# Kernel tuning notes

Measured on AMD Instinct MI355X. Metric: run time of the kernel, lower is better.

The kernel has to match this reference:

```python
import jax, jax.numpy as jnp
import numpy as np

B, N, N_IN, MSG_HID, MSG_OUT, N_HID, N_OUT, K = 32, 128, 16, 64, 64, 64, 16, 4
E = N * (N - 1)  # 16256 directed edges, fully connected w/o self-loops


def setup_inputs() -> dict:
    key = jax.random.key(0)
    ks = jax.random.split(key, 8)
    # one-hot relation matrices (NRI convention)
    rows, cols = np.where(np.ones((N, N)) - np.eye(N))
    eye = np.eye(N, dtype=np.float32)
    rel_rec = jnp.asarray(eye[rows])   # [E, N]
    rel_send = jnp.asarray(eye[cols])  # [E, N]
    s = 0.1  # weight init scale
    return {
        "inputs": jax.random.normal(ks[0], (B, N_IN, N), jnp.float32),
        "rel_rec": rel_rec,
        "rel_send": rel_send,
        "rel_types": jax.nn.softmax(jax.random.normal(ks[1], (B, E, K), jnp.float32), axis=-1),
        "W1": jax.random.normal(ks[2], (K, 2 * N_IN, MSG_HID), jnp.float32) * s,
        "b1": jnp.zeros((K, MSG_HID), jnp.float32),
        "W2": jax.random.normal(ks[3], (K, MSG_HID, MSG_OUT), jnp.float32) * s,
        "b2": jnp.zeros((K, MSG_OUT), jnp.float32),
        "Wo1": jax.random.normal(ks[4], (MSG_OUT + N_IN, N_HID), jnp.float32) * s,
        "bo1": jnp.zeros((N_HID,), jnp.float32),
        "Wo2": jax.random.normal(ks[5], (N_HID, N_HID), jnp.float32) * s,
        "bo2": jnp.zeros((N_HID,), jnp.float32),
        "Wo3": jax.random.normal(ks[6], (N_HID, N_OUT), jnp.float32) * s,
        "bo3": jnp.zeros((N_OUT,), jnp.float32),
    }


def reference(inputs, rel_rec, rel_send, rel_types, W1, b1, W2, b2, Wo1, bo1, Wo2, bo2, Wo3, bo3):
    x = jnp.transpose(inputs, (0, 2, 1))                     # [B, N, n_in]
    senders = jnp.einsum('en,bnf->bef', rel_send, x)          # [B, E, n_in]
    receivers = jnp.einsum('en,bnf->bef', rel_rec, x)         # [B, E, n_in]
    pre_msg = jnp.concatenate([senders, receivers], axis=-1)  # [B, E, 2*n_in]
    all_msgs = jnp.zeros((pre_msg.shape[0], pre_msg.shape[1], W2.shape[-1]), pre_msg.dtype)
    for k in range(W1.shape[0]):  # small fixed loop over edge types
        m = jax.nn.relu(pre_msg @ W1[k] + b1[k])
        m = jax.nn.relu(m @ W2[k] + b2[k])
        all_msgs = all_msgs + m * rel_types[:, :, k:k + 1]
    # edge2node aggregation (no normalization in forward path, matches source)
    agg_msgs = jnp.einsum('bem,en->bnm', all_msgs, rel_rec)   # [B, N, msg_out]
    aug_msgs = jnp.concatenate([x, agg_msgs], axis=-1)        # [B, N, n_in+msg_out]
    h = jax.nn.relu(aug_msgs @ Wo1 + bo1)  # dropout disabled (eval mode)
    h = jax.nn.relu(h @ Wo2 + bo2)
    pred = h @ Wo3 + bo3                                      # [B, N, n_out]
    return jnp.transpose(pred, (0, 2, 1))                     # [B, n_out, N]
```

## Files before the change

kernel.cpp:

```cpp
#include <hip/hip_runtime.h>
#include <stdint.h>

#define B_  32
#define N_  128
#define NIN 16
#define K_  4
#define E_  (N_*(N_-1))

typedef float f4   __attribute__((ext_vector_type(4)));
typedef short bf8  __attribute__((ext_vector_type(8)));

static __device__ __forceinline__ unsigned short f2bf(float f) {
    union { float f; unsigned u; } v; v.f = f;
    unsigned r = v.u + 0x7FFFu + ((v.u >> 16) & 1u);
    return (unsigned short)(r >> 16);
}
static __device__ __forceinline__ float bf2f(unsigned short h) {
    union { unsigned u; float f; } v; v.u = ((unsigned)h) << 16;
    return v.f;
}

__global__ __launch_bounds__(256) void precompute_sr(
    const float* __restrict__ inp, const float* __restrict__ W1,
    const float* __restrict__ b1,
    unsigned short* __restrict__ Sb, unsigned short* __restrict__ Rb)
{
    int gid = blockIdx.x * 256 + threadIdx.x;
    int c = gid & 63;
    int n = (gid >> 6) & 127;
    int b = (gid >> 13) & 31;
    int k = gid >> 18;
    float s = 0.f, r = 0.f;
    const float* w1s = W1 + (k*32)*64 + c;
    const float* w1r = W1 + (k*32 + 16)*64 + c;
    const float* xp  = inp + (b*NIN)*N_ + n;
    #pragma unroll
    for (int f = 0; f < 16; ++f) {
        float xv = xp[f*N_];
        s += xv * w1s[f*64];
        r += xv * w1r[f*64];
    }
    r += b1[k*64 + c];
    Sb[gid] = f2bf(s);
    Rb[gid] = f2bf(r);
}

__global__ __launch_bounds__(256) void pack_w2(
    const float* __restrict__ W2, unsigned short* __restrict__ w2b)
{
    int t = blockIdx.x * 256 + threadIdx.x;
    int i    = t & 7;
    int lane = (t >> 3) & 63;
    int nt   = (t >> 9) & 3;
    int ks   = (t >> 11) & 1;
    int k    = t >> 12;
    int c = ks*32 + (lane >> 4)*8 + i;
    int o = nt*16 + (lane & 15);
    w2b[t] = f2bf(W2[(k*64 + c)*64 + o]);
}

__global__ __launch_bounds__(256) void edge_node(
    const unsigned short* __restrict__ Sb,
    const unsigned short* __restrict__ Rb,
    const unsigned short* __restrict__ w2b,
    const float* __restrict__ inp,
    const float* __restrict__ rt,
    const float* __restrict__ b2,
    const float* __restrict__ Wo1, const float* __restrict__ bo1,
    const float* __restrict__ Wo2, const float* __restrict__ bo2,
    const float* __restrict__ Wo3, const float* __restrict__ bo3,
    float* __restrict__ out)
{
    __shared__ float aggK[4*64];
    __shared__ float aug[80];
    __shared__ float h1s[64];
    __shared__ float h2s[64];

    const int tid  = threadIdx.x;
    const int r    = blockIdx.x & 127;
    const int b    = blockIdx.x >> 7;
    const int k    = tid >> 6;
    const int lane = tid & 63;
    const int col  = lane & 15;
    const int q    = lane >> 4;

    if (tid < 16) aug[tid] = inp[(b*NIN + tid)*N_ + r];

    const bf8* w2v = (const bf8*)w2b;
    bf8 w2f[2][4];
    #pragma unroll
    for (int ks = 0; ks < 2; ++ks)
        #pragma unroll
        for (int nt = 0; nt < 4; ++nt)
            w2f[ks][nt] = w2v[((k*2 + ks)*4 + nt)*64 + lane];

    const bf8* Sv = (const bf8*)Sb;
    const bf8* Rv = (const bf8*)Rb;
    const int rowbaseR = ((k*B_ + b)*N_ + r) * 8;
    float rf[2][8];
    #pragma unroll
    for (int ks = 0; ks < 2; ++ks) {
        bf8 rv = Rv[rowbaseR + ks*4 + q];
        #pragma unroll
        for (int i = 0; i < 8; ++i) rf[ks][i] = bf2f((unsigned short)rv[i]);
    }

    float b2v[4];
    #pragma unroll
    for (int nt = 0; nt < 4; ++nt) b2v[nt] = b2[k*64 + nt*16 + col];

    float aggacc[4] = {0.f, 0.f, 0.f, 0.f};
    const int rowbaseS = (k*B_ + b)*N_*8;
    const int ebase    = b*E_ + r*127;

    for (int mt = 0; mt < 8; ++mt) {
        int j = mt*16 + col;
        int s = j + (j >= r ? 1 : 0);
        if (s > 127) s = 127;
        bf8 h1f[2];
        #pragma unroll
        for (int ks = 0; ks < 2; ++ks) {
            bf8 sv = Sv[rowbaseS + s*8 + ks*4 + q];
            bf8 h;
            #pragma unroll
            for (int i = 0; i < 8; ++i) {
                float v = bf2f((unsigned short)sv[i]) + rf[ks][i];
                h[i] = (short)f2bf(fmaxf(v, 0.f));
            }
            h1f[ks] = h;
        }
        f4 acc[4];
        #pragma unroll
        for (int nt = 0; nt < 4; ++nt) {
            f4 z = {0.f, 0.f, 0.f, 0.f};
            acc[nt] = __builtin_amdgcn_mfma_f32_16x16x32_bf16(h1f[0], w2f[0][nt], z, 0, 0, 0);
            acc[nt] = __builtin_amdgcn_mfma_f32_16x16x32_bf16(h1f[1], w2f[1][nt], acc[nt], 0, 0, 0);
        }
        float rtv[4];
        #pragma unroll
        for (int i = 0; i < 4; ++i) {
            int jrow = mt*16 + q*4 + i;
            rtv[i] = (jrow < 127) ? rt[(ebase + jrow)*4 + k] : 0.f;
        }
        #pragma unroll
        for (int nt = 0; nt < 4; ++nt)
            #pragma unroll
            for (int i = 0; i < 4; ++i)
                aggacc[nt] += rtv[i] * fmaxf(acc[nt][i] + b2v[nt], 0.f);
    }

    #pragma unroll
    for (int nt = 0; nt < 4; ++nt) {
        float v = aggacc[nt];
        v += __shfl_xor(v, 16, 64);
        v += __shfl_xor(v, 32, 64);
        if (lane < 16) aggK[k*64 + nt*16 + lane] = v;
    }
    __syncthreads();

    if (tid < 64) {
        float a = aggK[tid] + aggK[64 + tid] + aggK[128 + tid] + aggK[192 + tid];
        aug[16 + tid] = a;
    }
    __syncthreads();
    if (tid < 64) {
        float accv = bo1[tid];
        #pragma unroll 8
        for (int i = 0; i < 80; ++i) accv += aug[i] * Wo1[i*64 + tid];
        h1s[tid] = fmaxf(accv, 0.f);
    }
    __syncthreads();
    if (tid < 64) {
        float accv = bo2[tid];
        #pragma unroll 8
        for (int i = 0; i < 64; ++i) accv += h1s[i] * Wo2[i*64 + tid];
        h2s[tid] = fmaxf(accv, 0.f);
    }
    __syncthreads();
    if (tid < 16) {
        float accv = bo3[tid];
        #pragma unroll 8
        for (int i = 0; i < 64; ++i) accv += h2s[i] * Wo3[i*16 + tid];
        out[(b*NIN + tid)*N_ + r] = accv;
    }
}

extern "C" void kernel_launch(void* const* d_in, const int* in_sizes, int n_in,
                              void* d_out, int out_size, void* d_ws, size_t ws_size,
                              hipStream_t stream)
{
    const float* inp = (const float*)d_in[0];
    const float* rt  = (const float*)d_in[3];
    const float* W1  = (const float*)d_in[4];
    const float* b1  = (const float*)d_in[5];
    const float* W2  = (const float*)d_in[6];
    const float* b2  = (const float*)d_in[7];
    const float* Wo1 = (const float*)d_in[8];
    const float* bo1 = (const float*)d_in[9];
    const float* Wo2 = (const float*)d_in[10];
    const float* bo2 = (const float*)d_in[11];
    const float* Wo3 = (const float*)d_in[12];
    const float* bo3 = (const float*)d_in[13];

    unsigned short* Sb  = (unsigned short*)d_ws;
    unsigned short* Rb  = Sb + (1u << 20);
    unsigned short* w2b = Rb + (1u << 20);

    hipLaunchKernelGGL(precompute_sr, dim3(4096), dim3(256), 0, stream,
                       inp, W1, b1, Sb, Rb);
    hipLaunchKernelGGL(pack_w2, dim3(64), dim3(256), 0, stream, W2, w2b);
    hipLaunchKernelGGL(edge_node, dim3(B_*N_), dim3(256), 0, stream,
                       Sb, Rb, w2b, inp, rt, b2,
                       Wo1, bo1, Wo2, bo2, Wo3, bo3, (float*)d_out);
}
```

Before: 166.2 us.

## Switch to fp16 MFMA, fuse prep kernels, transpose rel_types, split node MLP

```diff
diff --git a/kernel.cpp b/kernel.cpp
--- a/kernel.cpp
+++ b/kernel.cpp
@@ -7,65 +7,63 @@
 #define K_  4
 #define E_  (N_*(N_-1))
 
-typedef float f4   __attribute__((ext_vector_type(4)));
-typedef short bf8  __attribute__((ext_vector_type(8)));
-
-static __device__ __forceinline__ unsigned short f2bf(float f) {
-    union { float f; unsigned u; } v; v.f = f;
-    unsigned r = v.u + 0x7FFFu + ((v.u >> 16) & 1u);
-    return (unsigned short)(r >> 16);
+typedef float    f4 __attribute__((ext_vector_type(4)));
+typedef _Float16 h8 __attribute__((ext_vector_type(8)));
+
+__global__ __launch_bounds__(256) void prep(
+    const float* __restrict__ inp, const float* __restrict__ W1,
+    const float* __restrict__ b1,  const float* __restrict__ W2,
+    const float* __restrict__ rt,
+    _Float16* __restrict__ Sh, _Float16* __restrict__ Rh,
+    _Float16* __restrict__ w2h, float* __restrict__ rtp)
+{
+    const int bid = blockIdx.x;
+    const int tid = threadIdx.x;
+    if (bid < 4096) {
+        int gid = bid*256 + tid;
+        int c = gid & 63;
+        int n = (gid >> 6) & 127;
+        int b = (gid >> 13) & 31;
+        int k = gid >> 18;
+        float s = 0.f, r = 0.f;
+        const float* w1s = W1 + (k*32)*64 + c;
+        const float* w1r = W1 + (k*32 + 16)*64 + c;
+        const float* xp  = inp + (b*NIN)*N_ + n;
+        #pragma unroll
+        for (int f = 0; f < 16; ++f) {
+            float xv = xp[f*N_];
+            s += xv * w1s[f*64];
+            r += xv * w1r[f*64];
+        }
+        r += b1[k*64 + c];
+        Sh[gid] = (_Float16)s;
+        Rh[gid] = (_Float16)r;
+    } else if (bid < 4160) {
+        int t = (bid - 4096)*256 + tid;
+        int i    = t & 7;
+        int lane = (t >> 3) & 63;
+        int nt   = (t >> 9) & 3;
+        int ks   = (t >> 11) & 1;
+        int k    = t >> 12;
+        int c = ks*32 + (lane >> 4)*8 + i;
+        int o = nt*16 + (lane & 15);
+        w2h[t] = (_Float16)W2[(k*64 + c)*64 + o];
+    } else {
+        int t = (bid - 4160)*256 + tid;
+        int j = t & 127;
+        int r = (t >> 7) & 127;
+        int b = (t >> 14) & 31;
+        int k = t >> 19;
+        float v = 0.f;
+        if (j < 127) v = rt[(b*E_ + r*127 + j)*4 + k];
+        rtp[t] = v;
+    }
 }
-static __device__ __forceinline__ float bf2f(unsigned short h) {
-    union { unsigned u; float f; } v; v.u = ((unsigned)h) << 16;
-    return v.f;
-}
-
-__global__ __launch_bounds__(256) void precompute_sr(
-    const float* __restrict__ inp, const float* __restrict__ W1,
-    const float* __restrict__ b1,
-    unsigned short* __restrict__ Sb, unsigned short* __restrict__ Rb)
-{
-    int gid = blockIdx.x * 256 + threadIdx.x;
-    int c = gid & 63;
-    int n = (gid >> 6) & 127;
-    int b = (gid >> 13) & 31;
-    int k = gid >> 18;
-    float s = 0.f, r = 0.f;
-    const float* w1s = W1 + (k*32)*64 + c;
-    const float* w1r = W1 + (k*32 + 16)*64 + c;
-    const float* xp  = inp + (b*NIN)*N_ + n;
-    #pragma unroll
-    for (int f = 0; f < 16; ++f) {
-        float xv = xp[f*N_];
-        s += xv * w1s[f*64];
-        r += xv * w1r[f*64];
-    }
-    r += b1[k*64 + c];
-    Sb[gid] = f2bf(s);
-    Rb[gid] = f2bf(r);
-}
-
-__global__ __launch_bounds__(256) void pack_w2(
-    const float* __restrict__ W2, unsigned short* __restrict__ w2b)
-{
-    int t = blockIdx.x * 256 + threadIdx.x;
-    int i    = t & 7;
-    int lane = (t >> 3) & 63;
-    int nt   = (t >> 9) & 3;
-    int ks   = (t >> 11) & 1;
-    int k    = t >> 12;
-    int c = ks*32 + (lane >> 4)*8 + i;
-    int o = nt*16 + (lane & 15);
-    w2b[t] = f2bf(W2[(k*64 + c)*64 + o]);
-}
 
 __global__ __launch_bounds__(256) void edge_node(
-    const unsigned short* __restrict__ Sb,
-    const unsigned short* __restrict__ Rb,
-    const unsigned short* __restrict__ w2b,
-    const float* __restrict__ inp,
-    const float* __restrict__ rt,
-    const float* __restrict__ b2,
+    const _Float16* __restrict__ Sh, const _Float16* __restrict__ Rh,
+    const _Float16* __restrict__ w2h, const float* __restrict__ rtp,
+    const float* __restrict__ inp, const float* __restrict__ b2,
     const float* __restrict__ Wo1, const float* __restrict__ bo1,
     const float* __restrict__ Wo2, const float* __restrict__ bo2,
     const float* __restrict__ Wo3, const float* __restrict__ bo3,
@@ -73,6 +71,7 @@
 {
     __shared__ float aggK[4*64];
     __shared__ float aug[80];
+    __shared__ float psum[4][64];
     __shared__ float h1s[64];
     __shared__ float h2s[64];
 
@@ -86,67 +85,52 @@
 
     if (tid < 16) aug[tid] = inp[(b*NIN + tid)*N_ + r];
 
-    const bf8* w2v = (const bf8*)w2b;
-    bf8 w2f[2][4];
+    const h8* w2v = (const h8*)w2h;
+    h8 w2f[2][4];
     #pragma unroll
     for (int ks = 0; ks < 2; ++ks)
         #pragma unroll
         for (int nt = 0; nt < 4; ++nt)
             w2f[ks][nt] = w2v[((k*2 + ks)*4 + nt)*64 + lane];
 
-    const bf8* Sv = (const bf8*)Sb;
-    const bf8* Rv = (const bf8*)Rb;
-    const int rowbaseR = ((k*B_ + b)*N_ + r) * 8;
-    float rf[2][8];
-    #pragma unroll
-    for (int ks = 0; ks < 2; ++ks) {
-        bf8 rv = Rv[rowbaseR + ks*4 + q];
-        #pragma unroll
-        for (int i = 0; i < 8; ++i) rf[ks][i] = bf2f((unsigned short)rv[i]);
-    }
-
-    float b2v[4];
-    #pragma unroll
-    for (int nt = 0; nt < 4; ++nt) b2v[nt] = b2[k*64 + nt*16 + col];
+    const h8* Sv = (const h8*)Sh;
+    const h8* Rv = (const h8*)Rh;
+    const int rowR = ((k*B_ + b)*N_ + r) * 8;
+    h8 rf0 = Rv[rowR + q];
+    h8 rf1 = Rv[rowR + 4 + q];
+
+    f4 b2i[4];
+    #pragma unroll
+    for (int nt = 0; nt < 4; ++nt) {
+        float v = b2[k*64 + nt*16 + col];
+        b2i[nt][0] = v; b2i[nt][1] = v; b2i[nt][2] = v; b2i[nt][3] = v;
+    }
 
     float aggacc[4] = {0.f, 0.f, 0.f, 0.f};
-    const int rowbaseS = (k*B_ + b)*N_*8;
-    const int ebase    = b*E_ + r*127;
-
+    const int rowSbase = (k*B_ + b)*N_*8;
+    const float* rtrow = rtp + ((k*B_ + b)*N_ + r)*128;
+    const h8 zero8 = {0,0,0,0,0,0,0,0};
+
+    #pragma unroll
     for (int mt = 0; mt < 8; ++mt) {
         int j = mt*16 + col;
         int s = j + (j >= r ? 1 : 0);
         if (s > 127) s = 127;
-        bf8 h1f[2];
-        #pragma unroll
-        for (int ks = 0; ks < 2; ++ks) {
-            bf8 sv = Sv[rowbaseS + s*8 + ks*4 + q];
-            bf8 h;
-            #pragma unroll
-            for (int i = 0; i < 8; ++i) {
-                float v = bf2f((unsigned short)sv[i]) + rf[ks][i];
-                h[i] = (short)f2bf(fmaxf(v, 0.f));
-            }
-            h1f[ks] = h;
-        }
-        f4 acc[4];
+        h8 a0 = Sv[rowSbase + s*8 + q]     + rf0;
+        h8 a1 = Sv[rowSbase + s*8 + 4 + q] + rf1;
+        a0 = __builtin_elementwise_max(a0, zero8);
+        a1 = __builtin_elementwise_max(a1, zero8);
+
+        f4 rtv = *(const f4*)(rtrow + mt*16 + q*4);
+
         #pragma unroll
         for (int nt = 0; nt < 4; ++nt) {
-            f4 z = {0.f, 0.f, 0.f, 0.f};
-            acc[nt] = __builtin_amdgcn_mfma_f32_16x16x32_bf16(h1f[0], w2f[0][nt], z, 0, 0, 0);
-            acc[nt] = __builtin_amdgcn_mfma_f32_16x16x32_bf16(h1f[1], w2f[1][nt], acc[nt], 0, 0, 0);
-        }
-        float rtv[4];
-        #pragma unroll
-        for (int i = 0; i < 4; ++i) {
-            int jrow = mt*16 + q*4 + i;
-            rtv[i] = (jrow < 127) ? rt[(ebase + jrow)*4 + k] : 0.f;
-        }
-        #pragma unroll
-        for (int nt = 0; nt < 4; ++nt)
+            f4 acc = __builtin_amdgcn_mfma_f32_16x16x32_f16(a0, w2f[0][nt], b2i[nt], 0, 0, 0);
+            acc     = __builtin_amdgcn_mfma_f32_16x16x32_f16(a1, w2f[1][nt], acc,    0, 0, 0);
             #pragma unroll
             for (int i = 0; i < 4; ++i)
-                aggacc[nt] += rtv[i] * fmaxf(acc[nt][i] + b2v[nt], 0.f);
+                aggacc[nt] += rtv[i] * fmaxf(acc[i], 0.f);
+        }
     }
 
     #pragma unroll
@@ -158,31 +142,45 @@
     }
     __syncthreads();
 
+    if (tid < 64)
+        aug[16 + tid] = aggK[tid] + aggK[64 + tid] + aggK[128 + tid] + aggK[192 + tid];
+    __syncthreads();
+
+    {
+        int o = tid & 63, p = tid >> 6;
+        float s = 0.f;
+        #pragma unroll
+        for (int i = p*20; i < p*20 + 20; ++i) s += aug[i] * Wo1[i*64 + o];
+        psum[p][o] = s;
+    }
+    __syncthreads();
+    if (tid < 64)
+        h1s[tid] = fmaxf(psum[0][tid] + psum[1][tid] + psum[2][tid] + psum[3][tid] + bo1[tid], 0.f);
+    __syncthreads();
+
+    {
+        int o = tid & 63, p = tid >> 6;
+        float s = 0.f;
+        #pragma unroll
+        for (int i = p*16; i < p*16 + 16; ++i) s += h1s[i] * Wo2[i*64 + o];
+        psum[p][o] = s;
+    }
+    __syncthreads();
+    if (tid < 64)
+        h2s[tid] = fmaxf(psum[0][tid] + psum[1][tid] + psum[2][tid] + psum[3][tid] + bo2[tid], 0.f);
+    __syncthreads();
+
     if (tid < 64) {
-        float a = aggK[tid] + aggK[64 + tid] + aggK[128 + tid] + aggK[192 + tid];
-        aug[16 + tid] = a;
-    }
-    __syncthreads();
-    if (tid < 64) {
-        float accv = bo1[tid];
-        #pragma unroll 8
-        for (int i = 0; i < 80; ++i) accv += aug[i] * Wo1[i*64 + tid];
-        h1s[tid] = fmaxf(accv, 0.f);
-    }
-    __syncthreads();
-    if (tid < 64) {
-        float accv = bo2[tid];
-        #pragma unroll 8
-        for (int i = 0; i < 64; ++i) accv += h1s[i] * Wo2[i*64 + tid];
-        h2s[tid] = fmaxf(accv, 0.f);
-    }
-    __syncthreads();
-    if (tid < 16) {
-        float accv = bo3[tid];
-        #pragma unroll 8
-        for (int i = 0; i < 64; ++i) accv += h2s[i] * Wo3[i*16 + tid];
-        out[(b*NIN + tid)*N_ + r] = accv;
-    }
+        int o = tid & 15, p = tid >> 4;
+        float s = 0.f;
+        #pragma unroll
+        for (int i = p*16; i < p*16 + 16; ++i) s += h2s[i] * Wo3[i*16 + o];
+        psum[p][o] = s;
+    }
+    __syncthreads();
+    if (tid < 16)
+        out[(b*NIN + tid)*N_ + r] =
+            psum[0][tid] + psum[1][tid] + psum[2][tid] + psum[3][tid] + bo3[tid];
 }
 
 extern "C" void kernel_launch(void* const* d_in, const int* in_sizes, int n_in,
@@ -202,14 +200,14 @@
     const float* Wo3 = (const float*)d_in[12];
     const float* bo3 = (const float*)d_in[13];
 
-    unsigned short* Sb  = (unsigned short*)d_ws;
-    unsigned short* Rb  = Sb + (1u << 20);
-    unsigned short* w2b = Rb + (1u << 20);
-
-    hipLaunchKernelGGL(precompute_sr, dim3(4096), dim3(256), 0, stream,
-                       inp, W1, b1, Sb, Rb);
-    hipLaunchKernelGGL(pack_w2, dim3(64), dim3(256), 0, stream, W2, w2b);
+    _Float16* Sh  = (_Float16*)d_ws;
+    _Float16* Rh  = Sh + (1u << 20);
+    _Float16* w2h = Rh + (1u << 20);
+    float*    rtp = (float*)(w2h + 16384);
+
+    hipLaunchKernelGGL(prep, dim3(12352), dim3(256), 0, stream,
+                       inp, W1, b1, W2, rt, Sh, Rh, w2h, rtp);
     hipLaunchKernelGGL(edge_node, dim3(B_*N_), dim3(256), 0, stream,
-                       Sb, Rb, w2b, inp, rt, b2,
+                       Sh, Rh, w2h, rtp, inp, b2,
                        Wo1, bo1, Wo2, bo2, Wo3, bo3, (float*)d_out);
 }
```

New measurement: 164.7 us. No clear change (-0.9%).
